# Kernel optimization log

Hardware: AMD Instinct MI355X
Metric: run time of the kernel (lower is better)

## Reference

```python
import jax, jax.numpy as jnp
import numpy as np

EPS = 1.1920929e-07  # torch RMSNorm default eps = finfo(float32).eps


def segsum(a):
    # a: (..., T) -> (..., T, T); [i, j] = sum_{j < t <= i} a[t] for j <= i, -inf above diag
    T = a.shape[-1]
    cs = jnp.cumsum(a, axis=-1)
    diff = cs[..., :, None] - cs[..., None, :]
    mask = jnp.tril(jnp.ones((T, T), dtype=bool))
    return jnp.where(mask, diff, -jnp.inf)


def dw_causal_conv(x, w):
    # x: (B, L, C), w: (C, K) depthwise causal conv (left pad K-1), matches Conv1d(pad=K-1)[:, :L]
    K = w.shape[-1]
    L = x.shape[1]
    xp = jnp.pad(x, ((0, 0), (K - 1, 0), (0, 0)))
    out = jnp.zeros_like(x)
    for j in range(K):
        out = out + xp[:, j:j + L, :] * w[:, j]
    return out


def ssd(X, A, Bv, Cv, block_len, init_state):
    # X: (B,L,H,P) pre-multiplied by dt; A: (B,L,H) = A*dt; Bv/Cv: (B,L,H,N)
    Bsz, L, H, P = X.shape
    N = Bv.shape[-1]
    c = L // block_len
    Xb = X.reshape(Bsz, c, block_len, H, P)
    Bb = Bv.reshape(Bsz, c, block_len, H, N)
    Cb = Cv.reshape(Bsz, c, block_len, H, N)
    Ab = A.reshape(Bsz, c, block_len, H).transpose(0, 3, 1, 2)  # (B,H,c,l)
    A_cumsum = jnp.cumsum(Ab, axis=-1)
    Ltri = jnp.exp(segsum(Ab))  # (B,H,c,l,l)
    # intra-chunk (diagonal block) output
    Y_diag = jnp.einsum('bclhn,bcshn,bhcls,bcshp->bclhp', Cb, Bb, Ltri, Xb)
    # per-chunk final states
    decay_states = jnp.exp(A_cumsum[..., -1:] - A_cumsum)  # (B,H,c,l)
    states = jnp.einsum('bclhn,bhcl,bclhp->bchpn', Bb, decay_states, Xb)
    states = jnp.concatenate([init_state[:, None], states], axis=1)  # (B,c+1,H,P,N)
    # inter-chunk recurrence via segsum over chunk boundaries
    last_A = A_cumsum[..., -1]  # (B,H,c)
    decay_chunk = jnp.exp(segsum(jnp.pad(last_A, ((0, 0), (0, 0), (1, 0)))))  # (B,H,c+1,c+1)
    new_states = jnp.einsum('bhzc,bchpn->bzhpn', decay_chunk, states)
    states, final_state = new_states[:, :-1], new_states[:, -1]
    # off-diagonal contribution from carried-in states
    state_decay_out = jnp.exp(A_cumsum)  # (B,H,c,l)
    Y_off = jnp.einsum('bclhn,bchpn,bhcl->bclhp', Cb, states, state_decay_out)
    Y = (Y_diag + Y_off).reshape(Bsz, L, H, P)
    return Y, final_state


def setup_inputs():
    key = jax.random.key(0)
    ks = jax.random.split(key, 8)
    d_model, d_state, d_conv, expand, headdim, ngroups = 1024, 128, 4, 2, 64, 1
    d_inner = expand * d_model                      # 2048
    H = d_inner // headdim                          # 32
    proj_out = 2 * d_inner + 2 * ngroups * d_state + H  # 4384
    conv_dim = d_inner + 2 * ngroups * d_state      # 2304
    B, L = 2, 2048
    x = jax.random.normal(ks[0], (B, L, d_model), dtype=jnp.float32)
    state = jnp.zeros((B, H, headdim, d_state), dtype=jnp.float32)
    in_proj_w = jax.random.normal(ks[1], (proj_out, d_model), dtype=jnp.float32) * 0.02
    conv_w = jax.random.normal(ks[2], (conv_dim, d_conv), dtype=jnp.float32) * 0.2
    A_log = jnp.log(jax.random.uniform(ks[3], (H,), minval=1.0, maxval=16.0))
    dt0 = jnp.exp(jax.random.uniform(ks[4], (H,)) * (np.log(0.1) - np.log(0.001)) + np.log(0.001))
    dt0 = jnp.maximum(dt0, 0.0001)
    dt_bias = dt0 + jnp.log(-jnp.expm1(-dt0))
    D_param = jnp.ones((H,), dtype=jnp.float32)
    norm_w = jnp.ones((d_inner,), dtype=jnp.float32)
    out_proj_w = jax.random.normal(ks[5], (d_model, d_inner), dtype=jnp.float32) * 0.02
    return dict(x=x, state=state, in_proj_w=in_proj_w, conv_w=conv_w, A_log=A_log,
                dt_bias=dt_bias, D_param=D_param, norm_w=norm_w, out_proj_w=out_proj_w,
                block_len=64)


def reference(x, state, in_proj_w, conv_w, A_log, dt_bias, D_param, norm_w, out_proj_w, block_len):
    B, L, Dm = x.shape
    H = A_log.shape[0]
    P = state.shape[2]
    N = state.shape[3]
    d_inner = H * P
    conv_dim = conv_w.shape[0]
    zxbcdt = x @ in_proj_w.T  # (B,L,proj_out)
    z = zxbcdt[..., :d_inner]
    xBC = zxbcdt[..., d_inner:d_inner + conv_dim]
    dt = zxbcdt[..., d_inner + conv_dim:]
    xBC = jax.nn.silu(dw_causal_conv(xBC, conv_w))
    x_branch = xBC[..., :d_inner]
    Bv = xBC[..., d_inner:d_inner + N]           # ngroups = 1
    Cv = xBC[..., d_inner + N:]
    X = jax.nn.silu(x_branch.reshape(B, L, H, P))
    Bv = jnp.broadcast_to(jax.nn.silu(Bv)[:, :, None, :], (B, L, H, N))
    Cv = jnp.broadcast_to(jax.nn.silu(Cv)[:, :, None, :], (B, L, H, N))
    A = -jnp.exp(A_log)
    dt = jax.nn.softplus(dt + dt_bias)           # (B,L,H)
    A_dt = A * dt
    X_dt = X * dt[..., None]
    Y, final_state = ssd(X_dt, A_dt, Bv, Cv, block_len, state)
    Y = Y + D_param[None, None, :, None] * X
    y_flat = Y.reshape(B, L, d_inner)
    y_norm = y_flat * jax.lax.rsqrt(jnp.mean(y_flat * y_flat, axis=-1, keepdims=True) + EPS) * norm_w
    y_core = y_norm * jax.nn.sigmoid(z)
    y = y_core @ out_proj_w.T + x
    return (y, final_state)
```

## Files before the change

### kernel.cpp

```cpp
#include <hip/hip_runtime.h>
#include <math.h>

#define BATCH 2
#define LSEQ  2048
#define TTOK  4096
#define DM    1024
#define DI    2048
#define NH    32
#define HP    64
#define NS    128
#define CONVD 2304
#define PROJ  4384
#define NCH   32
#define BLK   64

typedef __bf16 bf16x8 __attribute__((ext_vector_type(8)));
typedef float  f32x4  __attribute__((ext_vector_type(4)));
typedef unsigned short ushortx8 __attribute__((ext_vector_type(8)));
typedef unsigned short ushort_t;
typedef __attribute__((address_space(3))) void  lds_void;
typedef __attribute__((address_space(1))) const void glb_cvoid;

__device__ __forceinline__ float silu_(float x) { return x / (1.f + __expf(-x)); }

__device__ __forceinline__ unsigned short f2bf(float x) {
    union { float f; unsigned u; } u; u.f = x;
    unsigned r = u.u + 0x7fffu + ((u.u >> 16) & 1u);
    return (unsigned short)(r >> 16);
}
__device__ __forceinline__ float bf2f(unsigned short s) {
    union { unsigned u; float f; } u; u.u = ((unsigned)s) << 16; return u.f;
}

__global__ __launch_bounds__(256)
void cast_all_k(const float* __restrict__ x, const float* __restrict__ ipw,
                const float* __restrict__ opw,
                ushort_t* __restrict__ xb, ushort_t* __restrict__ ipb,
                ushort_t* __restrict__ opb)
{
    const int n1 = TTOK*DM, n2 = PROJ*DM;
    int i = (blockIdx.x * 256 + threadIdx.x) * 8;
    const float* src; ushort_t* dst;
    if (i < n1)            { src = x   + i;             dst = xb  + i; }
    else if (i < n1 + n2)  { src = ipw + (i - n1);      dst = ipb + (i - n1); }
    else                   { src = opw + (i - n1 - n2); dst = opb + (i - n1 - n2); }
    float4 a = *(const float4*)(src);
    float4 b = *(const float4*)(src + 4);
    ushortx8 r;
    r[0]=f2bf(a.x); r[1]=f2bf(a.y); r[2]=f2bf(a.z); r[3]=f2bf(a.w);
    r[4]=f2bf(b.x); r[5]=f2bf(b.y); r[6]=f2bf(b.z); r[7]=f2bf(b.w);
    *(ushortx8*)dst = r;
}

template<int TM, int TN, int HASRES, int OUTBF>
__global__ __launch_bounds__(256)
void hgemm_nt(const ushort_t* __restrict__ A, const ushort_t* __restrict__ Bw,
              void* __restrict__ Cp, const float* __restrict__ R,
              int M, int N, int K)
{
    constexpr int JA = TM / 32, JB = TN / 32;
    constexpr int MT = TM / 32, NT = TN / 32;
    __shared__ ushort_t S[(TM + TN) * 64];
    ushort_t* As = S;
    ushort_t* Bs = S + TM * 64;
    char* As_c = (char*)As;
    char* Bs_c = (char*)Bs;
    const int t = threadIdx.x;
    const int l = t & 63, w = t >> 6;

    const int tx_ = (N + TN - 1) / TN, ty_ = (M + TM - 1) / TM;
    int bid = blockIdx.x;
    int sc = bid / (8 * ty_), rem = bid % (8 * ty_);
    int sw_w = min(8, tx_ - sc * 8);
    int bx = sc * 8 + rem % sw_w;
    int by = rem / sw_w;
    const int bm = by * TM, bn = bx * TN;
    const int wm = (w >> 1) * (TM / 2), wn = (w & 1) * (TN / 2);

    const int rowt = t >> 3;
    const int kkt  = (t & 7) * 8;
    const ushort_t* srcA = A + (size_t)(bm + rowt) * K + kkt;
    const ushort_t* srcB[JB];
#pragma unroll
    for (int j = 0; j < JB; ++j) {
        int gr = min(bn + j * 32 + rowt, N - 1);
        srcB[j] = Bw + (size_t)gr * K + kkt;
    }

    f32x4 acc[MT][NT] = {};
    const int fr = l & 15, sel8 = (l >> 4) * 8;

    for (int k0 = 0; k0 < K; k0 += 64) {
        __syncthreads();
#pragma unroll
        for (int j = 0; j < JA; ++j)
            __builtin_amdgcn_global_load_lds((glb_cvoid*)(srcA + (size_t)j * 32 * K + k0),
                                             (lds_void*)(As_c + 4096 * j + 16 * t), 16, 0, 0);
#pragma unroll
        for (int j = 0; j < JB; ++j)
            __builtin_amdgcn_global_load_lds((glb_cvoid*)(srcB[j] + k0),
                                             (lds_void*)(Bs_c + 4096 * j + 16 * t), 16, 0, 0);
        __syncthreads();
#pragma unroll
        for (int ks = 0; ks < 2; ++ks) {
            const int koff = ks * 32 + sel8;
            bf16x8 af[MT], bfr[NT];
#pragma unroll
            for (int mt = 0; mt < MT; ++mt)
                af[mt] = *(const bf16x8*)(As + (wm + mt * 16 + fr) * 64 + koff);
#pragma unroll
            for (int nt = 0; nt < NT; ++nt)
                bfr[nt] = *(const bf16x8*)(Bs + (wn + nt * 16 + fr) * 64 + koff);
#pragma unroll
            for (int mt = 0; mt < MT; ++mt)
#pragma unroll
                for (int nt = 0; nt < NT; ++nt)
                    acc[mt][nt] = __builtin_amdgcn_mfma_f32_16x16x32_bf16(af[mt], bfr[nt], acc[mt][nt], 0, 0, 0);
        }
    }

    const int crow = (l >> 4) * 4, ccol = l & 15;
#pragma unroll
    for (int mt = 0; mt < MT; ++mt) {
#pragma unroll
        for (int nt = 0; nt < NT; ++nt) {
            int n = bn + wn + nt * 16 + ccol;
            if (n >= N) continue;
#pragma unroll
            for (int i = 0; i < 4; ++i) {
                int m = bm + wm + mt * 16 + crow + i;
                float v = acc[mt][nt][i];
                if (HASRES) v += R[(size_t)m * N + n];
                if (OUTBF) ((ushort_t*)Cp)[(size_t)m * N + n] = f2bf(v);
                else       ((float*)Cp)[(size_t)m * N + n] = v;
            }
        }
    }
}

#define NCONVB 9216
__global__ __launch_bounds__(256)
void mid1_k(const ushort_t* __restrict__ zx, const float* __restrict__ cw,
            const float* __restrict__ dt_bias, const float* __restrict__ A_log,
            ushort_t* __restrict__ xBC, float* __restrict__ dt_sp, float* __restrict__ cumA)
{
    if (blockIdx.x < NCONVB) {
        int idx = blockIdx.x * 256 + threadIdx.x;
        int c4 = (idx % (CONVD/4)) * 4;
        int tkk = idx / (CONVD/4);
        int b = tkk >> 11, l = tkk & 2047;
        const ushort_t* col = zx + (size_t)b * LSEQ * PROJ + DI + c4;
        float4 w0 = *(const float4*)(cw + c4*4);
        float4 w1 = *(const float4*)(cw + c4*4 + 4);
        float4 w2 = *(const float4*)(cw + c4*4 + 8);
        float4 w3 = *(const float4*)(cw + c4*4 + 12);
        ushort4 tp = *(const ushort4*)(col + (size_t)l * PROJ);
        float a0 = w0.w * bf2f(tp.x), a1 = w1.w * bf2f(tp.y), a2 = w2.w * bf2f(tp.z), a3 = w3.w * bf2f(tp.w);
        if (l >= 1) { ushort4 v = *(const ushort4*)(col + (size_t)(l-1) * PROJ);
            a0 += w0.z*bf2f(v.x); a1 += w1.z*bf2f(v.y); a2 += w2.z*bf2f(v.z); a3 += w3.z*bf2f(v.w); }
        if (l >= 2) { ushort4 v = *(const ushort4*)(col + (size_t)(l-2) * PROJ);
            a0 += w0.y*bf2f(v.x); a1 += w1.y*bf2f(v.y); a2 += w2.y*bf2f(v.z); a3 += w3.y*bf2f(v.w); }
        if (l >= 3) { ushort4 v = *(const ushort4*)(col + (size_t)(l-3) * PROJ);
            a0 += w0.x*bf2f(v.x); a1 += w1.x*bf2f(v.y); a2 += w2.x*bf2f(v.z); a3 += w3.x*bf2f(v.w); }
        ushort4 o;
        o.x = f2bf(silu_(silu_(a0))); o.y = f2bf(silu_(silu_(a1)));
        o.z = f2bf(silu_(silu_(a2))); o.w = f2bf(silu_(silu_(a3)));
        *(ushort4*)(xBC + (size_t)tkk * CONVD + c4) = o;
    } else {
        int wid = (blockIdx.x - NCONVB) * 4 + (threadIdx.x >> 6);
        int ln = threadIdx.x & 63;
        int c = wid & 31, h = (wid >> 5) & 31, b = wid >> 10;
        int tk = b * LSEQ + c * BLK + ln;
        float xv = bf2f(zx[(size_t)tk * PROJ + (DI + CONVD) + h]) + dt_bias[h];
        float dtv = (xv > 20.f) ? xv : log1pf(__expf(xv));
        dt_sp[tk * NH + h] = dtv;
        float val = -__expf(A_log[h]) * dtv;
#pragma unroll
        for (int off = 1; off < 64; off <<= 1) {
            float u = __shfl_up(val, off, 64);
            if (ln >= off) val += u;
        }
        cumA[(size_t)wid * 64 + ln] = val;
    }
}

__global__ __launch_bounds__(256)
void mid2_k(const ushort_t* __restrict__ xBC, const float* __restrict__ dt_sp,
            const float* __restrict__ cumA, float* __restrict__ CBT,
            float* __restrict__ states)
{
    __shared__ __align__(16) char smem[33408];
    int t = threadIdx.x, r = t >> 2, q = t & 3;
    if (blockIdx.x < 64) {
        int b = blockIdx.x >> 5, c = blockIdx.x & 31;
        float (*sB)[65] = (float(*)[65])smem;
        float (*sC)[65] = sB + 64;
        const ushort_t* xb = xBC + (size_t)(b * LSEQ + c * BLK) * CONVD;
        float acc[16];
#pragma unroll
        for (int i = 0; i < 16; ++i) acc[i] = 0.f;
        for (int half = 0; half < 2; ++half) {
            __syncthreads();
#pragma unroll
            for (int jj = 0; jj < 4; ++jj) {
                ushort4 bv = *(const ushort4*)(xb + (size_t)r * CONVD + DI      + half*64 + q*16 + jj*4);
                ushort4 cv = *(const ushort4*)(xb + (size_t)r * CONVD + DI + NS + half*64 + q*16 + jj*4);
                int col = q*16 + jj*4;
                sB[r][col]=bf2f(bv.x); sB[r][col+1]=bf2f(bv.y); sB[r][col+2]=bf2f(bv.z); sB[r][col+3]=bf2f(bv.w);
                sC[r][col]=bf2f(cv.x); sC[r][col+1]=bf2f(cv.y); sC[r][col+2]=bf2f(cv.z); sC[r][col+3]=bf2f(cv.w);
            }
            __syncthreads();
            for (int n = 0; n < 64; ++n) {
                float cv = sC[r][n];
#pragma unroll
                for (int si = 0; si < 16; ++si)
                    acc[si] += cv * sB[q*16 + si][n];
            }
        }
        float* o = CBT + (size_t)blockIdx.x * 4096 + r * 64 + q * 16;
#pragma unroll
        for (int si = 0; si < 16; ++si) o[si] = acc[si];
    } else {
        int bi = blockIdx.x - 64;
        int h = bi & 31, c = (bi >> 5) & 31, b = bi >> 10;
        ushort_t* XdT = (ushort_t*)smem;
        ushort_t* BdT = XdT + 64 * 72;
        const float* cA = cumA + (size_t)((b*NH + h)*NCH + c) * 64;
        float scale = dt_sp[(b * LSEQ + c * BLK + r) * NH + h] * __expf(cA[63] - cA[r]);
        const ushort_t* xb = xBC + (size_t)(b * LSEQ + c * BLK + r) * CONVD;
#pragma unroll
        for (int jj = 0; jj < 4; ++jj) {
            ushort4 v = *(const ushort4*)(xb + h*HP + q*16 + jj*4);
            int p0 = q*16 + jj*4;
            XdT[(p0+0)*72 + r] = v.x; XdT[(p0+1)*72 + r] = v.y;
            XdT[(p0+2)*72 + r] = v.z; XdT[(p0+3)*72 + r] = v.w;
        }
#pragma unroll
        for (int jj = 0; jj < 8; ++jj) {
            ushort4 v = *(const ushort4*)(xb + DI + q*32 + jj*4);
            int n0 = q*32 + jj*4;
            BdT[(n0+0)*72 + r] = f2bf(bf2f(v.x)*scale);
            BdT[(n0+1)*72 + r] = f2bf(bf2f(v.y)*scale);
            BdT[(n0+2)*72 + r] = f2bf(bf2f(v.z)*scale);
            BdT[(n0+3)*72 + r] = f2bf(bf2f(v.w)*scale);
        }
        __syncthreads();
        int ln = t & 63, w = t >> 6;
        int wm = (w >> 1) * 32, wn = (w & 1) * 64;
        int fr = ln & 15;
        f32x4 acc[2][4] = {};
#pragma unroll
        for (int ks = 0; ks < 2; ++ks) {
            int koff = ks*32 + (ln >> 4) * 8;
            bf16x8 af[2], bv[4];
#pragma unroll
            for (int mt = 0; mt < 2; ++mt) af[mt] = *(const bf16x8*)&XdT[(wm + mt*16 + fr)*72 + koff];
#pragma unroll
            for (int nt = 0; nt < 4; ++nt) bv[nt] = *(const bf16x8*)&BdT[(wn + nt*16 + fr)*72 + koff];
#pragma unroll
            for (int mt = 0; mt < 2; ++mt)
#pragma unroll
                for (int nt = 0; nt < 4; ++nt)
                    acc[mt][nt] = __builtin_amdgcn_mfma_f32_16x16x32_bf16(af[mt], bv[nt], acc[mt][nt], 0, 0, 0);
        }
        float* o = states + (size_t)((b*NCH + c)*NH + h) * 8192;
        int crow = (ln >> 4) * 4, ccol = ln & 15;
#pragma unroll
        for (int mt = 0; mt < 2; ++mt)
#pragma unroll
            for (int nt = 0; nt < 4; ++nt)
#pragma unroll
                for (int i = 0; i < 4; ++i)
                    o[(wm + mt*16 + crow + i)*128 + wn + nt*16 + ccol] = acc[mt][nt][i];
    }
}

__global__ __launch_bounds__(256)
void scan_k(const float* __restrict__ init_state, const float* __restrict__ cumA,
            const float* __restrict__ states, ushort_t* __restrict__ pref,
            float* __restrict__ out_final)
{
    int idx = blockIdx.x * 256 + threadIdx.x;
    int h = (idx >> 13) & 31, b = idx >> 18;
    int pn = idx & 8191;
    float run = init_state[idx];
    const float* cAb = cumA + (size_t)(b*NH + h) * NCH * 64;
    for (int c = 0; c < NCH; ++c) {
        float la = cAb[c*64 + 63];
        size_t off = (size_t)((b*NCH + c)*NH + h) * 8192 + pn;
        float tmp = states[off];
        pref[off] = f2bf(run);
        run = expf(la) * run + tmp;
    }
    out_final[idx] = run;
}

__global__ __launch_bounds__(256)
void y_mfma_k(const ushort_t* __restrict__ xBC, const float* __restrict__ dt_sp,
              const float* __restrict__ cumA, const float* __restrict__ CBT,
              const ushort_t* __restrict__ pref, const float* __restrict__ D_param,
              ushort_t* __restrict__ Y)
{
    int bi = blockIdx.x;
    int h = bi & 31, c = (bi >> 5) & 31, b = bi >> 10;
    __shared__ ushort_t Wm[64 * 72];
    __shared__ ushort_t XT[64 * 72];
    __shared__ ushort_t Cd[64 * 136];
    __shared__ ushort_t Sp[64 * 136];
    __shared__ float sCA[64];
    __shared__ float sdt[64];
    int t = threadIdx.x, r = t >> 2, q = t & 3;
    const float* cA = cumA + (size_t)((b*NH + h)*NCH + c) * 64;
    if (t < 64) {
        sCA[t] = cA[t];
        sdt[t] = dt_sp[(b * LSEQ + c * BLK + t) * NH + h];
    }
    __syncthreads();
    size_t row = (size_t)(b * LSEQ + c * BLK + r);
    const ushort_t* xb = xBC + row * CONVD;
    float myA = sCA[r], eC = __expf(myA);
    const float* cbt = CBT + (size_t)(b*NCH + c) * 4096 + r * 64;
#pragma unroll
    for (int j = 0; j < 16; ++j) {
        int s = q*16 + j;
        float wv = (s <= r) ? cbt[s] * __expf(myA - sCA[s]) * sdt[s] : 0.f;
        Wm[r*72 + s] = f2bf(wv);
    }
#pragma unroll
    for (int jj = 0; jj < 4; ++jj) {
        ushort4 v = *(const ushort4*)(xb + h*HP + q*16 + jj*4);
        int p0 = q*16 + jj*4;
        XT[(p0+0)*72 + r] = v.x; XT[(p0+1)*72 + r] = v.y;
        XT[(p0+2)*72 + r] = v.z; XT[(p0+3)*72 + r] = v.w;
    }
#pragma unroll
    for (int jj = 0; jj < 8; ++jj) {
        ushort4 v = *(const ushort4*)(xb + DI + NS + q*32 + jj*4);
        int n0 = q*32 + jj*4;
        Cd[r*136 + n0+0] = f2bf(bf2f(v.x)*eC);
        Cd[r*136 + n0+1] = f2bf(bf2f(v.y)*eC);
        Cd[r*136 + n0+2] = f2bf(bf2f(v.z)*eC);
        Cd[r*136 + n0+3] = f2bf(bf2f(v.w)*eC);
    }
    const ushort_t* pr = pref + (size_t)((b*NCH + c)*NH + h) * 8192 + r * 128;
#pragma unroll
    for (int jj = 0; jj < 4; ++jj) {
        ushortx8 v = *(const ushortx8*)(pr + q*32 + jj*8);
        *(ushortx8*)&Sp[r*136 + q*32 + jj*8] = v;
    }
    __syncthreads();
    int ln = t & 63, w = t >> 6;
    int wm = (w >> 1) * 32, wn = (w & 1) * 32;
    int fr = ln & 15;
    f32x4 acc[2][2] = {};
#pragma unroll
    for (int ks = 0; ks < 2; ++ks) {
        int koff = ks*32 + (ln >> 4) * 8;
        bf16x8 af[2], bv[2];
#pragma unroll
        for (int mt = 0; mt < 2; ++mt) af[mt] = *(const bf16x8*)&Wm[(wm + mt*16 + fr)*72 + koff];
#pragma unroll
        for (int nt = 0; nt < 2; ++nt) bv[nt] = *(const bf16x8*)&XT[(wn + nt*16 + fr)*72 + koff];
#pragma unroll
        for (int mt = 0; mt < 2; ++mt)
#pragma unroll
            for (int nt = 0; nt < 2; ++nt)
                acc[mt][nt] = __builtin_amdgcn_mfma_f32_16x16x32_bf16(af[mt], bv[nt], acc[mt][nt], 0, 0, 0);
    }
#pragma unroll
    for (int ks = 0; ks < 4; ++ks) {
        int koff = ks*32 + (ln >> 4) * 8;
        bf16x8 af[2], bv[2];
#pragma unroll
        for (int mt = 0; mt < 2; ++mt) af[mt] = *(const bf16x8*)&Cd[(wm + mt*16 + fr)*136 + koff];
#pragma unroll
        for (int nt = 0; nt < 2; ++nt) bv[nt] = *(const bf16x8*)&Sp[(wn + nt*16 + fr)*136 + koff];
#pragma unroll
        for (int mt = 0; mt < 2; ++mt)
#pragma unroll
            for (int nt = 0; nt < 2; ++nt)
                acc[mt][nt] = __builtin_amdgcn_mfma_f32_16x16x32_bf16(af[mt], bv[nt], acc[mt][nt], 0, 0, 0);
    }
    float Dh = D_param[h];
    int crow = (ln >> 4) * 4, ccol = ln & 15;
#pragma unroll
    for (int mt = 0; mt < 2; ++mt)
#pragma unroll
        for (int nt = 0; nt < 2; ++nt)
#pragma unroll
            for (int i = 0; i < 4; ++i) {
                int li = wm + mt*16 + crow + i;
                int p  = wn + nt*16 + ccol;
                size_t rr = (size_t)(b*LSEQ + c*BLK + li);
                float xv = bf2f(xBC[rr * CONVD + h*HP + p]);
                Y[rr * DI + h*HP + p] = f2bf(acc[mt][nt][i] + Dh * xv);
            }
}

__global__ __launch_bounds__(256)
void rms_gate_k(const ushort_t* __restrict__ zx, const float* __restrict__ norm_w,
                const ushort_t* __restrict__ Y, ushort_t* __restrict__ Yb)
{
    int tk = blockIdx.x, t = threadIdx.x;
    const ushort_t* rowp = Y + (size_t)tk * DI + t*8;
    ushortx8 v = *(const ushortx8*)rowp;
    float f[8];
    float ss = 0.f;
#pragma unroll
    for (int i = 0; i < 8; ++i) { f[i] = bf2f(v[i]); ss += f[i]*f[i]; }
#pragma unroll
    for (int off = 32; off > 0; off >>= 1) ss += __shfl_xor(ss, off, 64);
    __shared__ float sw[4];
    __shared__ float stot;
    if ((t & 63) == 0) sw[t >> 6] = ss;
    __syncthreads();
    if (t == 0) stot = rsqrtf((sw[0]+sw[1]+sw[2]+sw[3]) * (1.f/DI) + 1.1920929e-07f);
    __syncthreads();
    float scale = stot;
    const ushort_t* zr = zx + (size_t)tk * PROJ + t*8;
    ushortx8 z = *(const ushortx8*)zr;
    float4 w0 = *(const float4*)(norm_w + t*8);
    float4 w1 = *(const float4*)(norm_w + t*8 + 4);
    float wv[8] = {w0.x,w0.y,w0.z,w0.w,w1.x,w1.y,w1.z,w1.w};
    ushortx8 o;
#pragma unroll
    for (int i = 0; i < 8; ++i)
        o[i] = f2bf(f[i]*scale*wv[i] / (1.f+__expf(-bf2f(z[i]))));
    *(ushortx8*)(Yb + (size_t)tk * DI + t*8) = o;
}

extern "C" void kernel_launch(void* const* d_in, const int* in_sizes, int n_in,
                              void* d_out, int out_size, void* d_ws, size_t ws_size,
                              hipStream_t stream)
{
    const float* x        = (const float*)d_in[0];
    const float* init_st  = (const float*)d_in[1];
    const float* in_proj  = (const float*)d_in[2];
    const float* conv_w   = (const float*)d_in[3];
    const float* A_log    = (const float*)d_in[4];
    const float* dt_bias  = (const float*)d_in[5];
    const float* D_param  = (const float*)d_in[6];
    const float* norm_w   = (const float*)d_in[7];
    const float* out_proj = (const float*)d_in[8];
    float* out = (float*)d_out;

    ushort_t* zx_bf  = (ushort_t*)d_ws;
    ushort_t* xBC_bf = zx_bf + (size_t)TTOK*PROJ;
    float* dt_sp  = (float*)(xBC_bf + (size_t)TTOK*CONVD);
    float* cumA   = dt_sp  + (size_t)TTOK*NH;
    float* CBTb   = cumA   + (size_t)TTOK*NH;
    float* states = CBTb   + 262144;
    ushort_t* pref = (ushort_t*)(states + 16777216);
    float* Yreg   = (float*)(pref + 16777216);
    ushort_t* opw_bf = (ushort_t*)(Yreg + (size_t)TTOK*DI);
    ushort_t* Y_bf   = (ushort_t*)Yreg;
    ushort_t* xb_bf  = (ushort_t*)Yreg;
    ushort_t* ipw_bf = xb_bf + (size_t)TTOK*DM;
    ushort_t* Yb_bf  = xBC_bf;

    const int nc = (TTOK*DM + PROJ*DM + DM*DI) / (256*8);
    cast_all_k<<<nc, 256, 0, stream>>>(x, in_proj, out_proj, xb_bf, ipw_bf, opw_bf);
    hgemm_nt<128,128,0,1><<<((PROJ+127)/128)*(TTOK/128), 256, 0, stream>>>(xb_bf, ipw_bf, zx_bf, nullptr, TTOK, PROJ, DM);
    mid1_k<<<NCONVB + BATCH*NH*NCH/4, 256, 0, stream>>>(zx_bf, conv_w, dt_bias, A_log, xBC_bf, dt_sp, cumA);
    mid2_k<<<64 + BATCH*NCH*NH, 256, 0, stream>>>(xBC_bf, dt_sp, cumA, CBTb, states);
    scan_k<<<(BATCH*NH*HP*NS)/256, 256, 0, stream>>>(init_st, cumA, states, pref, out + (size_t)TTOK*DM);
    y_mfma_k<<<BATCH*NCH*NH, 256, 0, stream>>>(xBC_bf, dt_sp, cumA, CBTb, pref, D_param, Y_bf);
    rms_gate_k<<<TTOK, 256, 0, stream>>>(zx_bf, norm_w, Y_bf, Yb_bf);
    hgemm_nt<128,64,1,0><<<(DM/64)*(TTOK/128), 256, 0, stream>>>(Yb_bf, opw_bf, out, x, TTOK, DM, DI);
}
```

Baseline: 338.4 us.

## Store chunk states in bf16 and split GEMM LDS tiles into k-halves

The per-chunk SSD states buffer is now written by mid2_k and read by scan_k as bf16 rather than fp32, which halves the traffic of this 64 MB intermediate. Separately, the GEMM's LDS staging is rearranged: each 64-wide k slab is stored as two 32-wide halves with 32-element rows, and each thread loads 4 threads per row instead of 8. This changes the LDS access pattern of the MFMA fragment reads, probably to reduce bank conflicts. The bf16 states add rounding error before the recurrence accumulates them.

```diff
diff --git a/kernel.cpp b/kernel.cpp
--- a/kernel.cpp
+++ b/kernel.cpp
@@ -58,8 +58,8 @@
               void* __restrict__ Cp, const float* __restrict__ R,
               int M, int N, int K)
 {
-    constexpr int JA = TM / 32, JB = TN / 32;
     constexpr int MT = TM / 32, NT = TN / 32;
+    constexpr int JA = TM / 64, JB = TN / 64;
     __shared__ ushort_t S[(TM + TN) * 64];
     ushort_t* As = S;
     ushort_t* Bs = S + TM * 64;
@@ -77,13 +77,13 @@
     const int bm = by * TM, bn = bx * TN;
     const int wm = (w >> 1) * (TM / 2), wn = (w & 1) * (TN / 2);
 
-    const int rowt = t >> 3;
-    const int kkt  = (t & 7) * 8;
+    const int rowt = t >> 2;
+    const int kkt  = (t & 3) * 8;
     const ushort_t* srcA = A + (size_t)(bm + rowt) * K + kkt;
     const ushort_t* srcB[JB];
 #pragma unroll
     for (int j = 0; j < JB; ++j) {
-        int gr = min(bn + j * 32 + rowt, N - 1);
+        int gr = min(bn + j * 64 + rowt, N - 1);
         srcB[j] = Bw + (size_t)gr * K + kkt;
     }
 
@@ -93,24 +93,26 @@
     for (int k0 = 0; k0 < K; k0 += 64) {
         __syncthreads();
 #pragma unroll
-        for (int j = 0; j < JA; ++j)
-            __builtin_amdgcn_global_load_lds((glb_cvoid*)(srcA + (size_t)j * 32 * K + k0),
-                                             (lds_void*)(As_c + 4096 * j + 16 * t), 16, 0, 0);
-#pragma unroll
-        for (int j = 0; j < JB; ++j)
-            __builtin_amdgcn_global_load_lds((glb_cvoid*)(srcB[j] + k0),
-                                             (lds_void*)(Bs_c + 4096 * j + 16 * t), 16, 0, 0);
+        for (int h = 0; h < 2; ++h) {
+#pragma unroll
+            for (int j = 0; j < JA; ++j)
+                __builtin_amdgcn_global_load_lds((glb_cvoid*)(srcA + (size_t)j * 64 * K + k0 + h * 32),
+                                                 (lds_void*)(As_c + h * TM * 64 + j * 4096 + 16 * t), 16, 0, 0);
+#pragma unroll
+            for (int j = 0; j < JB; ++j)
+                __builtin_amdgcn_global_load_lds((glb_cvoid*)(srcB[j] + k0 + h * 32),
+                                                 (lds_void*)(Bs_c + h * TN * 64 + j * 4096 + 16 * t), 16, 0, 0);
+        }
         __syncthreads();
 #pragma unroll
-        for (int ks = 0; ks < 2; ++ks) {
-            const int koff = ks * 32 + sel8;
+        for (int h = 0; h < 2; ++h) {
             bf16x8 af[MT], bfr[NT];
 #pragma unroll
             for (int mt = 0; mt < MT; ++mt)
-                af[mt] = *(const bf16x8*)(As + (wm + mt * 16 + fr) * 64 + koff);
+                af[mt] = *(const bf16x8*)(As + h * TM * 32 + (wm + mt * 16 + fr) * 32 + sel8);
 #pragma unroll
             for (int nt = 0; nt < NT; ++nt)
-                bfr[nt] = *(const bf16x8*)(Bs + (wn + nt * 16 + fr) * 64 + koff);
+                bfr[nt] = *(const bf16x8*)(Bs + h * TN * 32 + (wn + nt * 16 + fr) * 32 + sel8);
 #pragma unroll
             for (int mt = 0; mt < MT; ++mt)
 #pragma unroll
@@ -187,7 +189,7 @@
 __global__ __launch_bounds__(256)
 void mid2_k(const ushort_t* __restrict__ xBC, const float* __restrict__ dt_sp,
             const float* __restrict__ cumA, float* __restrict__ CBT,
-            float* __restrict__ states)
+            ushort_t* __restrict__ states)
 {
     __shared__ __align__(16) char smem[33408];
     int t = threadIdx.x, r = t >> 2, q = t & 3;
@@ -263,7 +265,7 @@
                 for (int nt = 0; nt < 4; ++nt)
                     acc[mt][nt] = __builtin_amdgcn_mfma_f32_16x16x32_bf16(af[mt], bv[nt], acc[mt][nt], 0, 0, 0);
         }
-        float* o = states + (size_t)((b*NCH + c)*NH + h) * 8192;
+        ushort_t* o = states + (size_t)((b*NCH + c)*NH + h) * 8192;
         int crow = (ln >> 4) * 4, ccol = ln & 15;
 #pragma unroll
         for (int mt = 0; mt < 2; ++mt)
@@ -271,13 +273,13 @@
             for (int nt = 0; nt < 4; ++nt)
 #pragma unroll
                 for (int i = 0; i < 4; ++i)
-                    o[(wm + mt*16 + crow + i)*128 + wn + nt*16 + ccol] = acc[mt][nt][i];
+                    o[(wm + mt*16 + crow + i)*128 + wn + nt*16 + ccol] = f2bf(acc[mt][nt][i]);
     }
 }
 
 __global__ __launch_bounds__(256)
 void scan_k(const float* __restrict__ init_state, const float* __restrict__ cumA,
-            const float* __restrict__ states, ushort_t* __restrict__ pref,
+            const ushort_t* __restrict__ states, ushort_t* __restrict__ pref,
             float* __restrict__ out_final)
 {
     int idx = blockIdx.x * 256 + threadIdx.x;
@@ -288,7 +290,7 @@
     for (int c = 0; c < NCH; ++c) {
         float la = cAb[c*64 + 63];
         size_t off = (size_t)((b*NCH + c)*NH + h) * 8192 + pn;
-        float tmp = states[off];
+        float tmp = bf2f(states[off]);
         pref[off] = f2bf(run);
         run = expf(la) * run + tmp;
     }
@@ -449,8 +451,8 @@
     float* dt_sp  = (float*)(xBC_bf + (size_t)TTOK*CONVD);
     float* cumA   = dt_sp  + (size_t)TTOK*NH;
     float* CBTb   = cumA   + (size_t)TTOK*NH;
-    float* states = CBTb   + 262144;
-    ushort_t* pref = (ushort_t*)(states + 16777216);
+    ushort_t* states = (ushort_t*)(CBTb + 262144);
+    ushort_t* pref = states + 16777216;
     float* Yreg   = (float*)(pref + 16777216);
     ushort_t* opw_bf = (ushort_t*)(Yreg + (size_t)TTOK*DI);
     ushort_t* Y_bf   = (ushort_t*)Yreg;
```

Result: faster. 297.7 us (-12.0%).
